# Kernel optimization log

Hardware: AMD Instinct MI355X
Metric: run time of the kernel (lower is better)

The kernel has to match this reference:

```python
import jax, jax.numpy as jnp
import numpy as np

N_NODES = 200000
N_EDGES = 240000
HIDDEN = 128
N_TYPES = 6


def setup_inputs() -> dict:
    key = jax.random.key(0)
    k1, k2, k3, k4, k5 = jax.random.split(key, 5)
    state_embedding = jax.random.normal(k1, (N_NODES, HIDDEN), dtype=jnp.float32)
    # row 0: edge type in [1, N_TYPES]; row 1: source node; row 2: target node
    etype = jax.random.randint(k2, (N_EDGES,), 1, N_TYPES + 1, dtype=jnp.int32)
    src = jax.random.randint(k3, (N_EDGES,), 0, N_NODES, dtype=jnp.int32)
    tgt = jax.random.randint(k4, (N_EDGES,), 0, N_NODES, dtype=jnp.int32)
    typed_edges = jnp.stack([etype, src, tgt], axis=0)  # [3, E]
    # stacked per-edge-type Linear(2H, H, bias=False) weights, applied as x @ W[t]
    W = jax.random.normal(k5, (N_TYPES, 2 * HIDDEN, HIDDEN), dtype=jnp.float32) / np.sqrt(2 * HIDDEN)
    return {"state_embedding": state_embedding, "typed_edges": typed_edges, "W": W}


def reference(state_embedding, typed_edges, W):
    etype, src, tgt = typed_edges[0], typed_edges[1], typed_edges[2]
    # gather source/target node states and concat -> [E, 2H]
    x = jnp.concatenate([state_embedding[src], state_embedding[tgt]], axis=1)
    n_types = W.shape[0]
    msgs = jnp.zeros((x.shape[0], W.shape[2]), dtype=x.dtype)
    # fixed small loop over edge types; masking replaces the dynamic boolean
    # filtering of the torch code (edges with type t use only W[t-1])
    for t in range(n_types):
        mask = (etype == t + 1)[:, None]
        msgs = msgs + jnp.where(mask, x @ W[t], jnp.zeros((), x.dtype))
    # scatter-add messages into target node slots, dim_size = num nodes
    return jax.ops.segment_sum(msgs, tgt, num_segments=state_embedding.shape[0])
```

## Files before the change

kernel.cpp:

```cpp
#include <hip/hip_runtime.h>

#define NTYPES 6
#define HID 128
#define E_TILE 64
#define TPB 4
#define BBUCK 64
#define NREG (NTYPES * BBUCK)
#define TNBITS 19
#define TNMASK ((1 << TNBITS) - 1)

typedef short short8 __attribute__((ext_vector_type(8)));
typedef float f32x4 __attribute__((ext_vector_type(4)));

static __device__ __forceinline__ ushort f2bf(float f) {
    union { float f; unsigned u; } v; v.f = f;
    unsigned r = v.u + 0x7FFFu + ((v.u >> 16) & 1u);
    return (ushort)(r >> 16);
}


__global__ void k_prep(int4* __restrict__ zp, int n4,
                       const float* __restrict__ Sf, ushort* __restrict__ Sb, int total,
                       const float* __restrict__ W, ushort* __restrict__ Wt,
                       int zb, int sb) {
    int b = blockIdx.x;
    if (b < zb) {
        int i = b * 256 + threadIdx.x;
        if (i < n4) zp[i] = make_int4(0, 0, 0, 0);
    } else if (b < zb + sb) {
        int g = ((b - zb) * 256 + threadIdx.x) * 8;
        if (g < total) {
            float4 a = *(const float4*)(Sf + g);
            float4 c = *(const float4*)(Sf + g + 4);
            ushort t[8] = { f2bf(a.x), f2bf(a.y), f2bf(a.z), f2bf(a.w),
                            f2bf(c.x), f2bf(c.y), f2bf(c.z), f2bf(c.w) };
            *(short8*)(Sb + g) = *(short8*)t;
        }
    } else {
        int t = (b - zb - sb) * 256 + threadIdx.x;
        int n  = t & 127;
        int k8 = (t >> 7) & 31;
        int ty = t >> 12;
        if (ty >= NTYPES) return;
        const float* wp = W + ((size_t)ty * 256 + (size_t)k8 * 8) * HID + n;
        ushort tmp[8];
        #pragma unroll
        for (int j = 0; j < 8; ++j) tmp[j] = f2bf(wp[(size_t)j * HID]);
        *(short8*)(Wt + ((size_t)ty * HID + n) * 256 + k8 * 8) = *(short8*)tmp;
    }
}

template <int RANK>
__global__ void k_bin(const int* __restrict__ etype, const int* __restrict__ src,
                      const int* __restrict__ tgt, int E, int CAP, int shift,
                      int* __restrict__ rcur, int* __restrict__ ncnt,
                      int2* __restrict__ sortedT2) {
    __shared__ int lcnt[NREG];
    __shared__ int lbase[NREG];
    for (int r = threadIdx.x; r < NREG; r += 256) lcnt[r] = 0;
    __syncthreads();
    int i = blockIdx.x * 256 + threadIdx.x;
    bool valid = (i < E);
    int sn = 0, pk = 0, reg = 0, lrk = 0;
    if (valid) {
        int t  = etype[i] - 1;
        int tn = tgt[i];
        sn = src[i];
        int a = 0;
        if (RANK) a = atomicAdd(&ncnt[tn], 1);
        pk  = tn | (a << TNBITS);
        reg = t * BBUCK + (tn >> shift);
        lrk = atomicAdd(&lcnt[reg], 1);
    }
    __syncthreads();
    for (int r = threadIdx.x; r < NREG; r += 256) {
        int c = lcnt[r];
        lbase[r] = c ? atomicAdd(&rcur[r], c) : 0;
    }
    __syncthreads();
    if (valid) {
        int pos = lbase[reg] + lrk;
        if (pos < CAP) sortedT2[(size_t)reg * CAP + pos] = make_int2(sn, pk);
    }
}

__global__ void k_scan1(const int* __restrict__ ncnt, int* __restrict__ noff,
                        int* __restrict__ bsum, int N) {
    __shared__ int s[256];
    const int b = blockIdx.x, t = threadIdx.x;
    const int base = b * 1024 + t * 4;
    int v[4];
    #pragma unroll
    for (int i = 0; i < 4; ++i) v[i] = (base + i < N) ? ncnt[base + i] : 0;
    int tsum = v[0] + v[1] + v[2] + v[3];
    s[t] = tsum;
    __syncthreads();
    for (int off = 1; off < 256; off <<= 1) {
        int x = (t >= off) ? s[t - off] : 0;
        __syncthreads();
        s[t] += x;
        __syncthreads();
    }
    if (t == 255) bsum[b] = s[255];
    int run = s[t] - tsum;
    #pragma unroll
    for (int i = 0; i < 4; ++i)
        if (base + i < N) { noff[base + i] = run; run += v[i]; }
}

__global__ void k_scan2(int* __restrict__ bsum, int nb) {
    __shared__ int s[256];
    const int t = threadIdx.x;
    int v = (t < nb) ? bsum[t] : 0;
    s[t] = v;
    __syncthreads();
    for (int off = 1; off < 256; off <<= 1) {
        int x = (t >= off) ? s[t - off] : 0;
        __syncthreads();
        s[t] += x;
        __syncthreads();
    }
    if (t < nb) bsum[t] = s[t] - v;
}

template <int MODE>
__launch_bounds__(256, 4)
__global__ void k_gemm(const ushort* __restrict__ Sb, const float* __restrict__ Sf,
                       const ushort* __restrict__ Wt, const int* __restrict__ rcur,
                       const int2* __restrict__ sortedT2, int CAP, int G,
                       const int* __restrict__ ncnt, const int* __restrict__ noff,
                       const int* __restrict__ bsum,
                       ushort* __restrict__ msgs, float* __restrict__ out) {
    __shared__ __align__(16) ushort Xs[E_TILE][264];
    __shared__ int sN[TPB][E_TILE];
    __shared__ int tN[TPB][E_TILE];
    __shared__ int dstR[TPB][E_TILE];

    int nwg = gridDim.x;
    int qq = nwg >> 3, rm = nwg & 7;
    int xcd = blockIdx.x & 7, io = blockIdx.x >> 3;
    int bid = (xcd < rm) ? xcd * (qq + 1) + io : rm * (qq + 1) + (xcd - rm) * qq + io;

    int reg = bid / G, g = bid - reg * G;
    int ty  = reg >> 6;
    int cnt_r = rcur[reg]; if (cnt_r > CAP) cnt_r = CAP;
    int nt  = (cnt_r + E_TILE - 1) >> 6;
    int ntl = nt - g * TPB;
    if (ntl <= 0) return;
    if (ntl > TPB) ntl = TPB;
    const int base = g * TPB * E_TILE;

    const int tid = threadIdx.x;
    const int w  = tid >> 6;
    const int l  = tid & 63;
    const int lr = l & 15;
    const int lg = l >> 4;

    {
        const int tt = tid >> 6, s = l;
        if (tt < ntl) {
            int gp = base + tt * E_TILE + s;
            int sn = 0, tn = 0, dr = 0;
            if (gp < cnt_r) {
                int2 v = sortedT2[(size_t)reg * CAP + gp];
                sn = v.x;
                tn = v.y & TNMASK;
                if (MODE == 2) {
                    int a = ((unsigned)v.y) >> TNBITS;
                    dr = (ncnt[tn] == 1) ? -(tn + 1)
                                         : (noff[tn] + bsum[tn >> 10] + a);
                }
            }
            sN[tt][s] = sn; tN[tt][s] = tn; dstR[tt][s] = dr;
        }
    }

    short8 wreg[16];
    {
        const ushort* wb = Wt + ((size_t)ty * HID + w * 32 + lr) * 256 + 8 * lg;
        #pragma unroll
        for (int kk = 0; kk < 8; ++kk) {
            wreg[2 * kk]     = *(const short8*)(wb + kk * 32);
            wreg[2 * kk + 1] = *(const short8*)(wb + 16 * 256 + kk * 32);
        }
    }
    __syncthreads();

    for (int tt = 0; tt < ntl; ++tt) {
        int cnt = cnt_r - (base + tt * E_TILE);
        if (cnt > E_TILE) cnt = E_TILE;

        {
            const int e = tid >> 2, q = tid & 3;
            ushort* dp = &Xs[e][q * 64];
            if (e < cnt) {
                const int node = (q & 2) ? tN[tt][e] : sN[tt][e];
                if (MODE == 2) {
                    const ushort* rp = Sb + (size_t)node * HID + (q & 1) * 64;
                    short8 v[8];
                    #pragma unroll
                    for (int i = 0; i < 8; ++i) v[i] = *(const short8*)(rp + i * 8);
                    #pragma unroll
                    for (int i = 0; i < 8; ++i) *(short8*)(dp + i * 8) = v[i];
                } else {
                    const float* rp = Sf + (size_t)node * HID + (q & 1) * 64;
                    #pragma unroll
                    for (int i = 0; i < 8; ++i) {
                        float4 a = *(const float4*)(rp + i * 8);
                        float4 b = *(const float4*)(rp + i * 8 + 4);
                        ushort tmp[8] = { f2bf(a.x), f2bf(a.y), f2bf(a.z), f2bf(a.w),
                                          f2bf(b.x), f2bf(b.y), f2bf(b.z), f2bf(b.w) };
                        *(short8*)(dp + i * 8) = *(short8*)tmp;
                    }
                }
            } else {
                short8 z = (short8){0, 0, 0, 0, 0, 0, 0, 0};
                #pragma unroll
                for (int i = 0; i < 8; ++i) *(short8*)(dp + i * 8) = z;
            }
        }
        __syncthreads();

        f32x4 acc[4][2];
        #pragma unroll
        for (int mf = 0; mf < 4; ++mf)
            #pragma unroll
            for (int nf = 0; nf < 2; ++nf)
                acc[mf][nf] = (f32x4){0.f, 0.f, 0.f, 0.f};

        const ushort* xb = &Xs[lr][8 * lg];
        #pragma unroll
        for (int kk = 0; kk < 8; ++kk) {
            const int k0 = kk * 32;
            #pragma unroll
            for (int mf = 0; mf < 4; ++mf) {
                short8 a = *(const short8*)(xb + mf * 16 * 264 + k0);
                acc[mf][0] = __builtin_amdgcn_mfma_f32_16x16x32_bf16(a, wreg[2 * kk],     acc[mf][0], 0, 0, 0);
                acc[mf][1] = __builtin_amdgcn_mfma_f32_16x16x32_bf16(a, wreg[2 * kk + 1], acc[mf][1], 0, 0, 0);
            }
        }
        __syncthreads();

        float (*Os)[132] = (float (*)[132])&Xs[0][0];
        #pragma unroll
        for (int mf = 0; mf < 4; ++mf)
            #pragma unroll
            for (int nf = 0; nf < 2; ++nf)
                #pragma unroll
                for (int r = 0; r < 4; ++r)
                    Os[mf * 16 + lg * 4 + r][w * 32 + nf * 16 + lr] = acc[mf][nf][r];
        __syncthreads();

        if (MODE == 2) {
            const int r8e = tid >> 4, cg = tid & 15;
            #pragma unroll
            for (int rr = 0; rr < 4; ++rr) {
                int row = rr * 16 + r8e;
                if (row < cnt) {
                    int dr = dstR[tt][row];
                    float4 a = *(const float4*)&Os[row][cg * 8];
                    float4 b = *(const float4*)&Os[row][cg * 8 + 4];
                    if (dr >= 0) {
                        ushort tmp[8] = { f2bf(a.x), f2bf(a.y), f2bf(a.z), f2bf(a.w),
                                          f2bf(b.x), f2bf(b.y), f2bf(b.z), f2bf(b.w) };
                        *(short8*)(msgs + (size_t)dr * HID + cg * 8) = *(short8*)tmp;
                    } else {
                        float* op = out + (size_t)(-dr - 1) * HID + cg * 8;
                        *(float4*)op = a;
                        *(float4*)(op + 4) = b;
                    }
                }
            }
        } else {
            const int rA = tid >> 7;
            const int c  = tid & (HID - 1);
            for (int it = 0; it < E_TILE / 2; ++it) {
                int ee = it * 2 + rA;
                if (ee < cnt) atomicAdd(&out[(size_t)tN[tt][ee] * HID + c], Os[ee][c]);
            }
        }
        __syncthreads();
    }
}

__launch_bounds__(256)
__global__ void k_scatter(const ushort* __restrict__ msgs, const int* __restrict__ noff,
                          const int* __restrict__ bsum, float* __restrict__ out,
                          int N, int Etot) {
    int node = blockIdx.x * 4 + (threadIdx.x >> 6);
    if (node >= N) return;
    int cp = threadIdx.x & 63;
    int s = noff[node] + bsum[node >> 10];
    int e = (node + 1 < N) ? (noff[node + 1] + bsum[(node + 1) >> 10]) : Etot;
    if (e - s == 1) return;
    float a0 = 0.f, a1 = 0.f;
    for (int r = s; r < e; ++r) {
        unsigned u = *(const unsigned*)(msgs + (size_t)r * HID + cp * 2);
        union { unsigned u; float f; } lo, hi;
        lo.u = u << 16; hi.u = u & 0xFFFF0000u;
        a0 += lo.f; a1 += hi.f;
    }
    *(float2*)(out + (size_t)node * HID + cp * 2) = make_float2(a0, a1);
}

extern "C" void kernel_launch(void* const* d_in, const int* in_sizes, int n_in,
                              void* d_out, int out_size, void* d_ws, size_t ws_size,
                              hipStream_t stream) {
    const float* Sf    = (const float*)d_in[0];
    const int*   edges = (const int*)d_in[1];
    const float* W     = (const float*)d_in[2];
    float* out = (float*)d_out;

    const int E = in_sizes[1] / 3;
    const int N = in_sizes[0] / HID;
    const int* etype = edges;
    const int* src   = edges + E;
    const int* tgt   = edges + 2 * E;
    int* ws = (int*)d_ws;

    int shift = 0;
    while (((N - 1) >> shift) >= BBUCK) shift++;
    const int nbuck = ((N - 1) >> shift) + 1;
    int mean = E / (NTYPES * nbuck); if (mean < 1) mean = 1;
    int CAP = ((mean + mean / 2 + 255) / 256) * 256; if (CAP < 256) CAP = 256;
    const int G = CAP >> 8;

    int* rcur = ws;
    int* ncnt = ws + NREG;
    int* noff = ncnt + N;
    int* bsum = noff + N + 1;
    size_t intsEnd = (size_t)(NREG + N + (N + 1) + 256) * sizeof(int);
    size_t st2Off  = (intsEnd + 255) & ~(size_t)255;
    size_t wtOff   = ((st2Off + (size_t)NREG * CAP * sizeof(int2)) + 255) & ~(size_t)255;
    size_t sbOff   = ((wtOff + (size_t)NTYPES * HID * 256 * 2) + 255) & ~(size_t)255;
    size_t msgsOff = ((sbOff + (size_t)N * HID * 2) + 255) & ~(size_t)255;
    size_t need2   = msgsOff + (size_t)E * HID * 2;

    const int nb1 = (N + 1023) / 1024;
    const int eb  = (E + 255) / 256;
    const int ngemm = NREG * G;
    ushort* Wt = (ushort*)((char*)d_ws + wtOff);
    int2* sortedT2 = (int2*)((char*)d_ws + st2Off);

    if (ws_size >= need2 && nb1 <= 256 && N < (1 << TNBITS)) {
        ushort* Sb   = (ushort*)((char*)d_ws + sbOff);
        ushort* msgs = (ushort*)((char*)d_ws + msgsOff);
        const int total = N * HID;
        const int n4 = (NREG + N + 3) / 4;
        const int zb = (n4 + 255) / 256;
        const int sb = (total / 8 + 255) / 256;
        const int wb = (NTYPES * HID * 32 + 255) / 256;

        k_prep<<<zb + sb + wb, 256, 0, stream>>>((int4*)ws, n4, Sf, Sb, total, W, Wt, zb, sb);
        k_bin<1><<<eb, 256, 0, stream>>>(etype, src, tgt, E, CAP, shift, rcur, ncnt, sortedT2);
        k_scan1<<<nb1, 256, 0, stream>>>(ncnt, noff, bsum, N);
        k_scan2<<<1, 256, 0, stream>>>(bsum, nb1);
        k_gemm<2><<<ngemm, 256, 0, stream>>>(Sb, Sf, Wt, rcur, sortedT2, CAP, G,
                                             ncnt, noff, bsum, msgs, out);
        k_scatter<<<(N + 3) / 4, 256, 0, stream>>>(msgs, noff, bsum, out, N, E);
    } else {
        const int n4 = (NREG + 3) / 4;
        k_prep<<<1 + (NTYPES * HID * 32 + 255) / 256, 256, 0, stream>>>(
            (int4*)ws, n4, nullptr, nullptr, 0, W, Wt, 1, 0);
        hipMemsetAsync(d_out, 0, (size_t)out_size * sizeof(float), stream);
        k_bin<0><<<eb, 256, 0, stream>>>(etype, src, tgt, E, CAP, shift, rcur, nullptr, sortedT2);
        k_gemm<0><<<ngemm, 256, 0, stream>>>(nullptr, Sf, Wt, rcur, sortedT2, CAP, G,
                                             nullptr, nullptr, nullptr, nullptr, out);
    }
}
```

Baseline: 153.8 us.

## Bin edges by type only and split gemm staging into K-halves

Edges are now binned only by edge type, not by type and target-node bucket. The gemm grid is built as a compact prefix over per-type tile counts, which removes the many empty or partially filled region blocks. The X staging tile is halved (source half then target half) and the epilogue is processed in two 32-row halves, which cuts shared memory per block to allow higher occupancy, at the cost of extra barriers. TPB drops to 2 to create more blocks, and the XCD block remapping is removed, which may reduce L2 locality for the target-sorted writes.

```diff
diff --git a/kernel.cpp b/kernel.cpp
--- a/kernel.cpp
+++ b/kernel.cpp
@@ -3,11 +3,10 @@
 #define NTYPES 6
 #define HID 128
 #define E_TILE 64
-#define TPB 4
-#define BBUCK 64
-#define NREG (NTYPES * BBUCK)
+#define TPB 2
 #define TNBITS 19
 #define TNMASK ((1 << TNBITS) - 1)
+#define XST 136
 
 typedef short short8 __attribute__((ext_vector_type(8)));
 typedef float f32x4 __attribute__((ext_vector_type(4)));
@@ -52,35 +51,34 @@
 
 template <int RANK>
 __global__ void k_bin(const int* __restrict__ etype, const int* __restrict__ src,
-                      const int* __restrict__ tgt, int E, int CAP, int shift,
-                      int* __restrict__ rcur, int* __restrict__ ncnt,
+                      const int* __restrict__ tgt, int E, int CAP,
+                      int* __restrict__ hdr, int* __restrict__ ncnt,
                       int2* __restrict__ sortedT2) {
-    __shared__ int lcnt[NREG];
-    __shared__ int lbase[NREG];
-    for (int r = threadIdx.x; r < NREG; r += 256) lcnt[r] = 0;
+    __shared__ int lcnt[NTYPES];
+    __shared__ int lbase[NTYPES];
+    if (threadIdx.x < NTYPES) lcnt[threadIdx.x] = 0;
     __syncthreads();
     int i = blockIdx.x * 256 + threadIdx.x;
     bool valid = (i < E);
-    int sn = 0, pk = 0, reg = 0, lrk = 0;
+    int sn = 0, pk = 0, t = 0, lrk = 0;
     if (valid) {
-        int t  = etype[i] - 1;
+        t  = etype[i] - 1;
         int tn = tgt[i];
         sn = src[i];
         int a = 0;
         if (RANK) a = atomicAdd(&ncnt[tn], 1);
         pk  = tn | (a << TNBITS);
-        reg = t * BBUCK + (tn >> shift);
-        lrk = atomicAdd(&lcnt[reg], 1);
-    }
-    __syncthreads();
-    for (int r = threadIdx.x; r < NREG; r += 256) {
-        int c = lcnt[r];
-        lbase[r] = c ? atomicAdd(&rcur[r], c) : 0;
+        lrk = atomicAdd(&lcnt[t], 1);
+    }
+    __syncthreads();
+    if (threadIdx.x < NTYPES) {
+        int c = lcnt[threadIdx.x];
+        lbase[threadIdx.x] = c ? atomicAdd(&hdr[16 + threadIdx.x], c) : 0;
     }
     __syncthreads();
     if (valid) {
-        int pos = lbase[reg] + lrk;
-        if (pos < CAP) sortedT2[(size_t)reg * CAP + pos] = make_int2(sn, pk);
+        int pos = lbase[t] + lrk;
+        if (pos < CAP) sortedT2[(size_t)t * CAP + pos] = make_int2(sn, pk);
     }
 }
 
@@ -126,29 +124,32 @@
 template <int MODE>
 __launch_bounds__(256, 4)
 __global__ void k_gemm(const ushort* __restrict__ Sb, const float* __restrict__ Sf,
-                       const ushort* __restrict__ Wt, const int* __restrict__ rcur,
-                       const int2* __restrict__ sortedT2, int CAP, int G,
+                       const ushort* __restrict__ Wt, const int* __restrict__ hdr,
+                       const int2* __restrict__ sortedT2, int CAP,
                        const int* __restrict__ ncnt, const int* __restrict__ noff,
                        const int* __restrict__ bsum,
                        ushort* __restrict__ msgs, float* __restrict__ out) {
-    __shared__ __align__(16) ushort Xs[E_TILE][264];
+    __shared__ __align__(16) ushort Xs[E_TILE][XST];
     __shared__ int sN[TPB][E_TILE];
     __shared__ int tN[TPB][E_TILE];
     __shared__ int dstR[TPB][E_TILE];
 
-    int nwg = gridDim.x;
-    int qq = nwg >> 3, rm = nwg & 7;
-    int xcd = blockIdx.x & 7, io = blockIdx.x >> 3;
-    int bid = (xcd < rm) ? xcd * (qq + 1) + io : rm * (qq + 1) + (xcd - rm) * qq + io;
-
-    int reg = bid / G, g = bid - reg * G;
-    int ty  = reg >> 6;
-    int cnt_r = rcur[reg]; if (cnt_r > CAP) cnt_r = CAP;
-    int nt  = (cnt_r + E_TILE - 1) >> 6;
-    int ntl = nt - g * TPB;
-    if (ntl <= 0) return;
-    if (ntl > TPB) ntl = TPB;
-    const int base = g * TPB * E_TILE;
+    int g = blockIdx.x;
+    int ty, t0 = 0, ntl = 0, cnt_t = 0;
+    for (ty = 0; ty < NTYPES; ++ty) {
+        int c = hdr[16 + ty];
+        if (c > CAP) c = CAP;
+        int nt = (c + E_TILE - 1) >> 6;
+        int ng = (nt + TPB - 1) / TPB;
+        if (g < ng) {
+            t0 = g * TPB;
+            ntl = nt - t0; if (ntl > TPB) ntl = TPB;
+            cnt_t = c;
+            break;
+        }
+        g -= ng;
+    }
+    if (ty == NTYPES) return;
 
     const int tid = threadIdx.x;
     const int w  = tid >> 6;
@@ -159,10 +160,10 @@
     {
         const int tt = tid >> 6, s = l;
         if (tt < ntl) {
-            int gp = base + tt * E_TILE + s;
+            int gp = (t0 + tt) * E_TILE + s;
             int sn = 0, tn = 0, dr = 0;
-            if (gp < cnt_r) {
-                int2 v = sortedT2[(size_t)reg * CAP + gp];
+            if (gp < cnt_t) {
+                int2 v = sortedT2[(size_t)ty * CAP + gp];
                 sn = v.x;
                 tn = v.y & TNMASK;
                 if (MODE == 2) {
@@ -186,40 +187,11 @@
     }
     __syncthreads();
 
+    const int e = tid >> 2, q = tid & 3;
+
     for (int tt = 0; tt < ntl; ++tt) {
-        int cnt = cnt_r - (base + tt * E_TILE);
+        int cnt = cnt_t - (t0 + tt) * E_TILE;
         if (cnt > E_TILE) cnt = E_TILE;
-
-        {
-            const int e = tid >> 2, q = tid & 3;
-            ushort* dp = &Xs[e][q * 64];
-            if (e < cnt) {
-                const int node = (q & 2) ? tN[tt][e] : sN[tt][e];
-                if (MODE == 2) {
-                    const ushort* rp = Sb + (size_t)node * HID + (q & 1) * 64;
-                    short8 v[8];
-                    #pragma unroll
-                    for (int i = 0; i < 8; ++i) v[i] = *(const short8*)(rp + i * 8);
-                    #pragma unroll
-                    for (int i = 0; i < 8; ++i) *(short8*)(dp + i * 8) = v[i];
-                } else {
-                    const float* rp = Sf + (size_t)node * HID + (q & 1) * 64;
-                    #pragma unroll
-                    for (int i = 0; i < 8; ++i) {
-                        float4 a = *(const float4*)(rp + i * 8);
-                        float4 b = *(const float4*)(rp + i * 8 + 4);
-                        ushort tmp[8] = { f2bf(a.x), f2bf(a.y), f2bf(a.z), f2bf(a.w),
-                                          f2bf(b.x), f2bf(b.y), f2bf(b.z), f2bf(b.w) };
-                        *(short8*)(dp + i * 8) = *(short8*)tmp;
-                    }
-                }
-            } else {
-                short8 z = (short8){0, 0, 0, 0, 0, 0, 0, 0};
-                #pragma unroll
-                for (int i = 0; i < 8; ++i) *(short8*)(dp + i * 8) = z;
-            }
-        }
-        __syncthreads();
 
         f32x4 acc[4][2];
         #pragma unroll
@@ -228,58 +200,96 @@
             for (int nf = 0; nf < 2; ++nf)
                 acc[mf][nf] = (f32x4){0.f, 0.f, 0.f, 0.f};
 
-        const ushort* xb = &Xs[lr][8 * lg];
-        #pragma unroll
-        for (int kk = 0; kk < 8; ++kk) {
-            const int k0 = kk * 32;
+        #pragma unroll
+        for (int half = 0; half < 2; ++half) {
+            {
+                ushort* dp = &Xs[e][q * 32];
+                if (e < cnt) {
+                    const int node = half ? tN[tt][e] : sN[tt][e];
+                    if (MODE == 2) {
+                        const ushort* rp = Sb + (size_t)node * HID + q * 32;
+                        #pragma unroll
+                        for (int i = 0; i < 4; ++i)
+                            *(short8*)(dp + i * 8) = *(const short8*)(rp + i * 8);
+                    } else {
+                        const float* rp = Sf + (size_t)node * HID + q * 32;
+                        #pragma unroll
+                        for (int i = 0; i < 4; ++i) {
+                            float4 a = *(const float4*)(rp + i * 8);
+                            float4 b = *(const float4*)(rp + i * 8 + 4);
+                            ushort tmp[8] = { f2bf(a.x), f2bf(a.y), f2bf(a.z), f2bf(a.w),
+                                              f2bf(b.x), f2bf(b.y), f2bf(b.z), f2bf(b.w) };
+                            *(short8*)(dp + i * 8) = *(short8*)tmp;
+                        }
+                    }
+                } else {
+                    short8 z = (short8){0, 0, 0, 0, 0, 0, 0, 0};
+                    #pragma unroll
+                    for (int i = 0; i < 4; ++i) *(short8*)(dp + i * 8) = z;
+                }
+            }
+            __syncthreads();
+
+            const ushort* xb = &Xs[lr][8 * lg];
             #pragma unroll
-            for (int mf = 0; mf < 4; ++mf) {
-                short8 a = *(const short8*)(xb + mf * 16 * 264 + k0);
-                acc[mf][0] = __builtin_amdgcn_mfma_f32_16x16x32_bf16(a, wreg[2 * kk],     acc[mf][0], 0, 0, 0);
-                acc[mf][1] = __builtin_amdgcn_mfma_f32_16x16x32_bf16(a, wreg[2 * kk + 1], acc[mf][1], 0, 0, 0);
-            }
-        }
-        __syncthreads();
+            for (int kk = 0; kk < 4; ++kk) {
+                const int k0 = kk * 32;
+                const int wi = 2 * (half * 4 + kk);
+                #pragma unroll
+                for (int mf = 0; mf < 4; ++mf) {
+                    short8 a = *(const short8*)(xb + mf * 16 * XST + k0);
+                    acc[mf][0] = __builtin_amdgcn_mfma_f32_16x16x32_bf16(a, wreg[wi],     acc[mf][0], 0, 0, 0);
+                    acc[mf][1] = __builtin_amdgcn_mfma_f32_16x16x32_bf16(a, wreg[wi + 1], acc[mf][1], 0, 0, 0);
+                }
+            }
+            __syncthreads();
+        }
 
         float (*Os)[132] = (float (*)[132])&Xs[0][0];
         #pragma unroll
-        for (int mf = 0; mf < 4; ++mf)
+        for (int h = 0; h < 2; ++h) {
             #pragma unroll
-            for (int nf = 0; nf < 2; ++nf)
+            for (int m2 = 0; m2 < 2; ++m2) {
+                const int mf = h * 2 + m2;
                 #pragma unroll
-                for (int r = 0; r < 4; ++r)
-                    Os[mf * 16 + lg * 4 + r][w * 32 + nf * 16 + lr] = acc[mf][nf][r];
-        __syncthreads();
-
-        if (MODE == 2) {
-            const int r8e = tid >> 4, cg = tid & 15;
-            #pragma unroll
-            for (int rr = 0; rr < 4; ++rr) {
-                int row = rr * 16 + r8e;
-                if (row < cnt) {
-                    int dr = dstR[tt][row];
-                    float4 a = *(const float4*)&Os[row][cg * 8];
-                    float4 b = *(const float4*)&Os[row][cg * 8 + 4];
-                    if (dr >= 0) {
-                        ushort tmp[8] = { f2bf(a.x), f2bf(a.y), f2bf(a.z), f2bf(a.w),
-                                          f2bf(b.x), f2bf(b.y), f2bf(b.z), f2bf(b.w) };
-                        *(short8*)(msgs + (size_t)dr * HID + cg * 8) = *(short8*)tmp;
-                    } else {
-                        float* op = out + (size_t)(-dr - 1) * HID + cg * 8;
-                        *(float4*)op = a;
-                        *(float4*)(op + 4) = b;
+                for (int nf = 0; nf < 2; ++nf)
+                    #pragma unroll
+                    for (int r = 0; r < 4; ++r)
+                        Os[m2 * 16 + lg * 4 + r][w * 32 + nf * 16 + lr] = acc[mf][nf][r];
+            }
+            __syncthreads();
+            if (MODE == 2) {
+                const int r8e = tid >> 4, cg = tid & 15;
+                #pragma unroll
+                for (int rr = 0; rr < 2; ++rr) {
+                    int rowl = rr * 16 + r8e;
+                    int row  = h * 32 + rowl;
+                    if (row < cnt) {
+                        int dr = dstR[tt][row];
+                        float4 a = *(const float4*)&Os[rowl][cg * 8];
+                        float4 b = *(const float4*)&Os[rowl][cg * 8 + 4];
+                        if (dr >= 0) {
+                            ushort tmp[8] = { f2bf(a.x), f2bf(a.y), f2bf(a.z), f2bf(a.w),
+                                              f2bf(b.x), f2bf(b.y), f2bf(b.z), f2bf(b.w) };
+                            *(short8*)(msgs + (size_t)dr * HID + cg * 8) = *(short8*)tmp;
+                        } else {
+                            float* op = out + (size_t)(-dr - 1) * HID + cg * 8;
+                            *(float4*)op = a;
+                            *(float4*)(op + 4) = b;
+                        }
                     }
                 }
-            }
-        } else {
-            const int rA = tid >> 7;
-            const int c  = tid & (HID - 1);
-            for (int it = 0; it < E_TILE / 2; ++it) {
-                int ee = it * 2 + rA;
-                if (ee < cnt) atomicAdd(&out[(size_t)tN[tt][ee] * HID + c], Os[ee][c]);
-            }
-        }
-        __syncthreads();
+            } else {
+                const int rA = tid >> 7;
+                const int c  = tid & (HID - 1);
+                for (int it = 0; it < 16; ++it) {
+                    int rowl = it * 2 + rA;
+                    int row  = h * 32 + rowl;
+                    if (row < cnt) atomicAdd(&out[(size_t)tN[tt][row] * HID + c], Os[rowl][c]);
+                }
+            }
+            __syncthreads();
+        }
     }
 }
 
@@ -318,27 +328,21 @@
     const int* tgt   = edges + 2 * E;
     int* ws = (int*)d_ws;
 
-    int shift = 0;
-    while (((N - 1) >> shift) >= BBUCK) shift++;
-    const int nbuck = ((N - 1) >> shift) + 1;
-    int mean = E / (NTYPES * nbuck); if (mean < 1) mean = 1;
-    int CAP = ((mean + mean / 2 + 255) / 256) * 256; if (CAP < 256) CAP = 256;
-    const int G = CAP >> 8;
-
-    int* rcur = ws;
-    int* ncnt = ws + NREG;
+    const int CAP = E / 5 + 4096;
+
+    int* ncnt = ws + 32;
     int* noff = ncnt + N;
     int* bsum = noff + N + 1;
-    size_t intsEnd = (size_t)(NREG + N + (N + 1) + 256) * sizeof(int);
+    size_t intsEnd = (size_t)(32 + N + (N + 1) + 256) * sizeof(int);
     size_t st2Off  = (intsEnd + 255) & ~(size_t)255;
-    size_t wtOff   = ((st2Off + (size_t)NREG * CAP * sizeof(int2)) + 255) & ~(size_t)255;
+    size_t wtOff   = ((st2Off + (size_t)NTYPES * CAP * sizeof(int2)) + 255) & ~(size_t)255;
     size_t sbOff   = ((wtOff + (size_t)NTYPES * HID * 256 * 2) + 255) & ~(size_t)255;
     size_t msgsOff = ((sbOff + (size_t)N * HID * 2) + 255) & ~(size_t)255;
     size_t need2   = msgsOff + (size_t)E * HID * 2;
 
     const int nb1 = (N + 1023) / 1024;
     const int eb  = (E + 255) / 256;
-    const int ngemm = NREG * G;
+    const int nblocks = (E + E_TILE * TPB - 1) / (E_TILE * TPB) + 2 * NTYPES;
     ushort* Wt = (ushort*)((char*)d_ws + wtOff);
     int2* sortedT2 = (int2*)((char*)d_ws + st2Off);
 
@@ -346,25 +350,30 @@
         ushort* Sb   = (ushort*)((char*)d_ws + sbOff);
         ushort* msgs = (ushort*)((char*)d_ws + msgsOff);
         const int total = N * HID;
-        const int n4 = (NREG + N + 3) / 4;
+        const int n4 = (32 + N + 3) / 4;
         const int zb = (n4 + 255) / 256;
         const int sb = (total / 8 + 255) / 256;
         const int wb = (NTYPES * HID * 32 + 255) / 256;
 
         k_prep<<<zb + sb + wb, 256, 0, stream>>>((int4*)ws, n4, Sf, Sb, total, W, Wt, zb, sb);
-        k_bin<1><<<eb, 256, 0, stream>>>(etype, src, tgt, E, CAP, shift, rcur, ncnt, sortedT2);
+        k_bin<1><<<eb, 256, 0, stream>>>(etype, src, tgt, E, CAP, ws, ncnt, sortedT2);
         k_scan1<<<nb1, 256, 0, stream>>>(ncnt, noff, bsum, N);
         k_scan2<<<1, 256, 0, stream>>>(bsum, nb1);
-        k_gemm<2><<<ngemm, 256, 0, stream>>>(Sb, Sf, Wt, rcur, sortedT2, CAP, G,
-                                             ncnt, noff, bsum, msgs, out);
+        k_gemm<2><<<nblocks, 256, 0, stream>>>(Sb, Sf, Wt, ws, sortedT2, CAP,
+                                               ncnt, noff, bsum, msgs, out);
         k_scatter<<<(N + 3) / 4, 256, 0, stream>>>(msgs, noff, bsum, out, N, E);
     } else {
-        const int n4 = (NREG + 3) / 4;
+        size_t wt0Off = ((32 * sizeof(int) + (size_t)NTYPES * CAP * sizeof(int2)) + 255) & ~(size_t)255;
+        int2* sortedT0 = (int2*)((char*)d_ws + ((32 * sizeof(int) + 255) & ~(size_t)255));
+        ushort* Wt0 = (ushort*)((char*)d_ws + wt0Off + 256);
+        sortedT0 = (int2*)((char*)d_ws + 256);
+        Wt0 = (ushort*)((char*)d_ws + 256 + (((size_t)NTYPES * CAP * sizeof(int2) + 255) & ~(size_t)255));
+
         k_prep<<<1 + (NTYPES * HID * 32 + 255) / 256, 256, 0, stream>>>(
-            (int4*)ws, n4, nullptr, nullptr, 0, W, Wt, 1, 0);
+            (int4*)ws, 8, nullptr, nullptr, 0, W, Wt0, 1, 0);
         hipMemsetAsync(d_out, 0, (size_t)out_size * sizeof(float), stream);
-        k_bin<0><<<eb, 256, 0, stream>>>(etype, src, tgt, E, CAP, shift, rcur, nullptr, sortedT2);
-        k_gemm<0><<<ngemm, 256, 0, stream>>>(nullptr, Sf, Wt, rcur, sortedT2, CAP, G,
-                                             nullptr, nullptr, nullptr, nullptr, out);
-    }
-}
+        k_bin<0><<<eb, 256, 0, stream>>>(etype, src, tgt, E, CAP, ws, nullptr, sortedT0);
+        k_gemm<0><<<nblocks, 256, 0, stream>>>(nullptr, Sf, Wt0, ws, sortedT0, CAP,
+                                               nullptr, nullptr, nullptr, nullptr, out);
+    }
+}
```

New measurement: 138.8 us. 9.7% less time.

## Replace fixed-capacity region bins with histogram-scanned compact tile layout

Applied to the files above, without the earlier changes.

Adds a histogram pass and a scan over the per-(type,bucket) region counts, so edges are placed into a compact, tile-aligned sorted array instead of fixed-capacity (CAP) per-region slots. The GEMM grid is now sized to the actual tile count, and each block binary-searches which region each of its tiles belongs to, reloading weights only when the type changes. This removes idle blocks and the possible dropping of edges when a region exceeds CAP. In exchange it adds two extra small kernel launches and a per-block search over the region offsets.

```diff
diff --git a/kernel.cpp b/kernel.cpp
--- a/kernel.cpp
+++ b/kernel.cpp
@@ -50,11 +50,41 @@
     }
 }
 
+__global__ void k_histA(const int* __restrict__ etype, const int* __restrict__ tgt,
+                        int E, int shift, int* __restrict__ rcnt) {
+    __shared__ int h[NREG];
+    for (int r = threadIdx.x; r < NREG; r += 256) h[r] = 0;
+    __syncthreads();
+    int i = blockIdx.x * 256 + threadIdx.x;
+    if (i < E) atomicAdd(&h[(etype[i] - 1) * BBUCK + (tgt[i] >> shift)], 1);
+    __syncthreads();
+    for (int r = threadIdx.x; r < NREG; r += 256) {
+        int c = h[r];
+        if (c) atomicAdd(&rcnt[r], c);
+    }
+}
+
+__global__ void k_scanR(const int* __restrict__ rcnt, int* __restrict__ rtile) {
+    __shared__ int s[NREG];
+    int t = threadIdx.x;
+    int tiles = (rcnt[t] + E_TILE - 1) >> 6;
+    s[t] = tiles;
+    __syncthreads();
+    for (int off = 1; off < NREG; off <<= 1) {
+        int x = (t >= off) ? s[t - off] : 0;
+        __syncthreads();
+        s[t] += x;
+        __syncthreads();
+    }
+    rtile[t] = s[t] - tiles;
+    if (t == NREG - 1) rtile[NREG] = s[NREG - 1];
+}
+
 template <int RANK>
-__global__ void k_bin(const int* __restrict__ etype, const int* __restrict__ src,
-                      const int* __restrict__ tgt, int E, int CAP, int shift,
-                      int* __restrict__ rcur, int* __restrict__ ncnt,
-                      int2* __restrict__ sortedT2) {
+__global__ void k_place(const int* __restrict__ etype, const int* __restrict__ src,
+                        const int* __restrict__ tgt, int E, int shift,
+                        const int* __restrict__ rtile, int* __restrict__ rcur,
+                        int* __restrict__ ncnt, int2* __restrict__ sortedT2) {
     __shared__ int lcnt[NREG];
     __shared__ int lbase[NREG];
     for (int r = threadIdx.x; r < NREG; r += 256) lcnt[r] = 0;
@@ -66,9 +96,12 @@
         int t  = etype[i] - 1;
         int tn = tgt[i];
         sn = src[i];
-        int a = 0;
-        if (RANK) a = atomicAdd(&ncnt[tn], 1);
-        pk  = tn | (a << TNBITS);
+        if (RANK) {
+            int a = atomicAdd(&ncnt[tn], 1);
+            pk = tn | (a << TNBITS);
+        } else {
+            pk = tn;
+        }
         reg = t * BBUCK + (tn >> shift);
         lrk = atomicAdd(&lcnt[reg], 1);
     }
@@ -79,8 +112,8 @@
     }
     __syncthreads();
     if (valid) {
-        int pos = lbase[reg] + lrk;
-        if (pos < CAP) sortedT2[(size_t)reg * CAP + pos] = make_int2(sn, pk);
+        int pos = (rtile[reg] << 6) + lbase[reg] + lrk;
+        sortedT2[pos] = make_int2(sn, pk);
     }
 }
 
@@ -126,8 +159,9 @@
 template <int MODE>
 __launch_bounds__(256, 4)
 __global__ void k_gemm(const ushort* __restrict__ Sb, const float* __restrict__ Sf,
-                       const ushort* __restrict__ Wt, const int* __restrict__ rcur,
-                       const int2* __restrict__ sortedT2, int CAP, int G,
+                       const ushort* __restrict__ Wt,
+                       const int* __restrict__ rcnt, const int* __restrict__ rtile_g,
+                       const int2* __restrict__ sortedT2,
                        const int* __restrict__ ncnt, const int* __restrict__ noff,
                        const int* __restrict__ bsum,
                        ushort* __restrict__ msgs, float* __restrict__ out) {
@@ -135,22 +169,22 @@
     __shared__ int sN[TPB][E_TILE];
     __shared__ int tN[TPB][E_TILE];
     __shared__ int dstR[TPB][E_TILE];
+    __shared__ int rtileL[NREG + 1];
+    __shared__ int tyA[TPB], cntA[TPB];
+
+    const int T = rtile_g[NREG];
 
     int nwg = gridDim.x;
     int qq = nwg >> 3, rm = nwg & 7;
     int xcd = blockIdx.x & 7, io = blockIdx.x >> 3;
     int bid = (xcd < rm) ? xcd * (qq + 1) + io : rm * (qq + 1) + (xcd - rm) * qq + io;
-
-    int reg = bid / G, g = bid - reg * G;
-    int ty  = reg >> 6;
-    int cnt_r = rcur[reg]; if (cnt_r > CAP) cnt_r = CAP;
-    int nt  = (cnt_r + E_TILE - 1) >> 6;
-    int ntl = nt - g * TPB;
-    if (ntl <= 0) return;
-    if (ntl > TPB) ntl = TPB;
-    const int base = g * TPB * E_TILE;
+    const int g0 = bid * TPB;
+    if (g0 >= T) return;
 
     const int tid = threadIdx.x;
+    for (int r = tid; r < NREG + 1; r += 256) rtileL[r] = rtile_g[r];
+    __syncthreads();
+
     const int w  = tid >> 6;
     const int l  = tid & 63;
     const int lr = l & 15;
@@ -158,13 +192,23 @@
 
     {
         const int tt = tid >> 6, s = l;
-        if (tt < ntl) {
-            int gp = base + tt * E_TILE + s;
+        const int gt = g0 + tt;
+        if (gt < T) {
+            int lo = 0, hi = NREG - 1;
+            while (lo < hi) {
+                int mid = (lo + hi + 1) >> 1;
+                if (rtileL[mid] <= gt) lo = mid; else hi = mid - 1;
+            }
+            const int reg = lo;
+            const int tIn = gt - rtileL[reg];
+            int cnt = rcnt[reg] - tIn * E_TILE;
+            if (cnt > E_TILE) cnt = E_TILE;
+            if (s == 0) { tyA[tt] = reg >> 6; cntA[tt] = cnt; }
             int sn = 0, tn = 0, dr = 0;
-            if (gp < cnt_r) {
-                int2 v = sortedT2[(size_t)reg * CAP + gp];
+            if (s < cnt) {
+                int2 v = sortedT2[(size_t)gt * E_TILE + s];
                 sn = v.x;
-                tn = v.y & TNMASK;
+                tn = (MODE == 2) ? (v.y & TNMASK) : v.y;
                 if (MODE == 2) {
                     int a = ((unsigned)v.y) >> TNBITS;
                     dr = (ncnt[tn] == 1) ? -(tn + 1)
@@ -172,23 +216,28 @@
                 }
             }
             sN[tt][s] = sn; tN[tt][s] = tn; dstR[tt][s] = dr;
-        }
-    }
+        } else if (s == 0) {
+            tyA[tt] = -1; cntA[tt] = -1;
+        }
+    }
+    __syncthreads();
 
     short8 wreg[16];
-    {
-        const ushort* wb = Wt + ((size_t)ty * HID + w * 32 + lr) * 256 + 8 * lg;
-        #pragma unroll
-        for (int kk = 0; kk < 8; ++kk) {
-            wreg[2 * kk]     = *(const short8*)(wb + kk * 32);
-            wreg[2 * kk + 1] = *(const short8*)(wb + 16 * 256 + kk * 32);
-        }
-    }
-    __syncthreads();
-
-    for (int tt = 0; tt < ntl; ++tt) {
-        int cnt = cnt_r - (base + tt * E_TILE);
-        if (cnt > E_TILE) cnt = E_TILE;
+    int tyCur = -1;
+
+    for (int tt = 0; tt < TPB; ++tt) {
+        const int cnt = cntA[tt];
+        if (cnt < 0) break;
+        const int ty = tyA[tt];
+        if (ty != tyCur) {
+            const ushort* wb = Wt + ((size_t)ty * HID + w * 32 + lr) * 256 + 8 * lg;
+            #pragma unroll
+            for (int kk = 0; kk < 8; ++kk) {
+                wreg[2 * kk]     = *(const short8*)(wb + kk * 32);
+                wreg[2 * kk + 1] = *(const short8*)(wb + 16 * 256 + kk * 32);
+            }
+            tyCur = ty;
+        }
 
         {
             const int e = tid >> 2, q = tid & 3;
@@ -320,25 +369,26 @@
 
     int shift = 0;
     while (((N - 1) >> shift) >= BBUCK) shift++;
-    const int nbuck = ((N - 1) >> shift) + 1;
-    int mean = E / (NTYPES * nbuck); if (mean < 1) mean = 1;
-    int CAP = ((mean + mean / 2 + 255) / 256) * 256; if (CAP < 256) CAP = 256;
-    const int G = CAP >> 8;
-
-    int* rcur = ws;
-    int* ncnt = ws + NREG;
-    int* noff = ncnt + N;
-    int* bsum = noff + N + 1;
-    size_t intsEnd = (size_t)(NREG + N + (N + 1) + 256) * sizeof(int);
+
+    const int SLOTS = E + NREG * E_TILE;
+
+    int* rcnt  = ws;
+    int* rcur  = ws + NREG;
+    int* ncnt  = ws + 2 * NREG;
+    int* rtile = ncnt + N;
+    int* noff  = rtile + NREG + 1;
+    int* bsum  = noff + N + 1;
+    size_t intsEnd = (size_t)(2 * NREG + N + (NREG + 1) + (N + 1) + 256) * sizeof(int);
     size_t st2Off  = (intsEnd + 255) & ~(size_t)255;
-    size_t wtOff   = ((st2Off + (size_t)NREG * CAP * sizeof(int2)) + 255) & ~(size_t)255;
+    size_t wtOff   = ((st2Off + (size_t)SLOTS * sizeof(int2)) + 255) & ~(size_t)255;
     size_t sbOff   = ((wtOff + (size_t)NTYPES * HID * 256 * 2) + 255) & ~(size_t)255;
     size_t msgsOff = ((sbOff + (size_t)N * HID * 2) + 255) & ~(size_t)255;
     size_t need2   = msgsOff + (size_t)E * HID * 2;
 
     const int nb1 = (N + 1023) / 1024;
     const int eb  = (E + 255) / 256;
-    const int ngemm = NREG * G;
+    const int Tmax = (E + E_TILE - 1) / E_TILE + NREG;
+    const int GB = (Tmax + TPB - 1) / TPB;
     ushort* Wt = (ushort*)((char*)d_ws + wtOff);
     int2* sortedT2 = (int2*)((char*)d_ws + st2Off);
 
@@ -346,25 +396,29 @@
         ushort* Sb   = (ushort*)((char*)d_ws + sbOff);
         ushort* msgs = (ushort*)((char*)d_ws + msgsOff);
         const int total = N * HID;
-        const int n4 = (NREG + N + 3) / 4;
+        const int n4 = (2 * NREG + N + 3) / 4;
         const int zb = (n4 + 255) / 256;
         const int sb = (total / 8 + 255) / 256;
         const int wb = (NTYPES * HID * 32 + 255) / 256;
 
         k_prep<<<zb + sb + wb, 256, 0, stream>>>((int4*)ws, n4, Sf, Sb, total, W, Wt, zb, sb);
-        k_bin<1><<<eb, 256, 0, stream>>>(etype, src, tgt, E, CAP, shift, rcur, ncnt, sortedT2);
+        k_histA<<<eb, 256, 0, stream>>>(etype, tgt, E, shift, rcnt);
+        k_scanR<<<1, NREG, 0, stream>>>(rcnt, rtile);
+        k_place<1><<<eb, 256, 0, stream>>>(etype, src, tgt, E, shift, rtile, rcur, ncnt, sortedT2);
         k_scan1<<<nb1, 256, 0, stream>>>(ncnt, noff, bsum, N);
         k_scan2<<<1, 256, 0, stream>>>(bsum, nb1);
-        k_gemm<2><<<ngemm, 256, 0, stream>>>(Sb, Sf, Wt, rcur, sortedT2, CAP, G,
-                                             ncnt, noff, bsum, msgs, out);
+        k_gemm<2><<<GB, 256, 0, stream>>>(Sb, Sf, Wt, rcnt, rtile, sortedT2,
+                                          ncnt, noff, bsum, msgs, out);
         k_scatter<<<(N + 3) / 4, 256, 0, stream>>>(msgs, noff, bsum, out, N, E);
     } else {
-        const int n4 = (NREG + 3) / 4;
+        const int n4 = (2 * NREG + 3) / 4;
         k_prep<<<1 + (NTYPES * HID * 32 + 255) / 256, 256, 0, stream>>>(
             (int4*)ws, n4, nullptr, nullptr, 0, W, Wt, 1, 0);
         hipMemsetAsync(d_out, 0, (size_t)out_size * sizeof(float), stream);
-        k_bin<0><<<eb, 256, 0, stream>>>(etype, src, tgt, E, CAP, shift, rcur, nullptr, sortedT2);
-        k_gemm<0><<<ngemm, 256, 0, stream>>>(nullptr, Sf, Wt, rcur, sortedT2, CAP, G,
-                                             nullptr, nullptr, nullptr, nullptr, out);
-    }
-}
+        k_histA<<<eb, 256, 0, stream>>>(etype, tgt, E, shift, rcnt);
+        k_scanR<<<1, NREG, 0, stream>>>(rcnt, rtile);
+        k_place<0><<<eb, 256, 0, stream>>>(etype, src, tgt, E, shift, rtile, rcur, nullptr, sortedT2);
+        k_gemm<0><<<GB, 256, 0, stream>>>(nullptr, Sf, Wt, rcnt, rtile, sortedT2,
+                                          nullptr, nullptr, nullptr, nullptr, out);
+    }
+}
```

Measured after the change: 168.7 us. +9.7%, slower.
